# Kernel optimization log

Hardware: AMD Instinct MI355X
Metric: run time of the kernel (lower is better)

Reference implementation:

```python
import jax, jax.numpy as jnp
import numpy as np

N, D = 8192, 128
NOISEVAR = 1.0

def _softplusinverse(v):
    return np.log(1.0 - np.exp(-v)) + v

def setup_inputs() -> dict:
    key = jax.random.key(0)
    kx, kn = jax.random.split(key)
    x = jax.random.normal(kx, (N, D), dtype=jnp.float32)
    noise = jax.random.normal(kn, (N, D), dtype=jnp.float32)
    phi = jnp.asarray(_softplusinverse(NOISEVAR), dtype=jnp.float32)
    return {"x": x, "phi": phi, "noise": noise}

def reference(x, phi, noise):
    # x: [n, d] encoded features; phi: scalar noise param; noise: [n, d] i.i.d. N(0,1)
    n = x.shape[0]
    var = jax.nn.softplus(phi)
    # Pairwise squared L2 distances via Gram-matrix trick (same math as
    # norm(x_i - x_j)^2, avoids the [n, n, d] broadcast intermediate).
    sq = jnp.sum(x * x, axis=1)                                  # [n]
    d2 = jnp.maximum(sq[:, None] + sq[None, :] - 2.0 * (x @ x.T), 0.0)  # [n, n]
    kde_contribution = jnp.mean(jax.nn.logsumexp(-0.5 * d2 / var, axis=1))
    IXT_nats = jnp.log(jnp.float32(n)) - kde_contribution
    IXT = IXT_nats / jnp.log(jnp.float32(2.0))  # bits=True -> nats2bits
    out = x + var * noise                        # training=True noise injection
    return out, IXT
```

## Files before the change

### kernel.cpp

```cpp
#include <hip/hip_runtime.h>

#define N 8192
#define D 128
#define T64 64
#define NT64 (N / T64)
#define NPAIR (NT64 * (NT64 + 1) / 2)
#define PREFIX 2176
#define TBASE(t) ((t) * NT64 - ((t) * ((t) - 1)) / 2)

typedef __attribute__((ext_vector_type(4))) int intx4;
typedef unsigned long long u64;

static __device__ inline float softplus_of(const float* __restrict__ phi) {
    float p = phi[0];
    return (p > 20.f) ? p : log1pf(__expf(p));
}


__global__ __launch_bounds__(256) void k1_prep(
        const float* __restrict__ x, const float* __restrict__ phi,
        const float* __restrict__ noise, float* __restrict__ out,
        signed char* __restrict__ q8, int* __restrict__ sqv,
        float* __restrict__ rowsum) {
    int tid = threadIdx.x;
    int gid = blockIdx.x * 256 + tid;
    int row = gid >> 4;
    int gc  = gid & 15;

    const float* xs = x + (size_t)row * D + gc * 8;
    float4 u = *(const float4*)xs, v = *(const float4*)(xs + 4);

    float f[8] = {u.x, u.y, u.z, u.w, v.x, v.y, v.z, v.w};
    u64 pack = 0;
    int s = 0;
    #pragma unroll
    for (int k = 0; k < 8; k++) {
        float c = fminf(fmaxf(f[k] * 16.f, -127.f), 127.f);
        int q = (int)rintf(c);
        s += q * q;
        pack |= ((u64)(q & 255)) << (8 * k);
    }
    *(u64*)&q8[(size_t)row * D + gc * 8] = pack;

    #pragma unroll
    for (int m = 1; m < 16; m <<= 1) s += __shfl_xor(s, m, 64);
    if (gc == 0) { sqv[row] = s; rowsum[row] = 0.f; }

    if (row >= PREFIX) {
        float var = softplus_of(phi);
        const float* ns = noise + (size_t)row * D + gc * 8;
        float4 nu = *(const float4*)ns, nv = *(const float4*)(ns + 4);
        float4 o0, o1;
        o0.x = u.x + var * nu.x; o0.y = u.y + var * nu.y;
        o0.z = u.z + var * nu.z; o0.w = u.w + var * nu.w;
        o1.x = v.x + var * nv.x; o1.y = v.y + var * nv.y;
        o1.z = v.z + var * nv.z; o1.w = v.w + var * nv.w;
        float* od = out + (size_t)row * D + gc * 8;
        *(float4*)od = o0; *(float4*)(od + 4) = o1;
    }
}

__global__ __launch_bounds__(256, 4) void k2_gram(
        const signed char* __restrict__ q8, const float* __restrict__ phi,
        const int* __restrict__ sqv, float* __restrict__ rowsum) {
    const int tid  = threadIdx.x;
    const int w    = blockIdx.x * 4 + (tid >> 6);
    const int lane = tid & 63;
    const int lrow = lane & 15;
    const int quad = lane >> 4;

    const float fm = (float)(2 * NT64 + 1);
    int ti = (int)((fm - sqrtf(fm * fm - 8.0f * (float)w)) * 0.5f);
    while (TBASE(ti + 1) <= w) ++ti;
    while (TBASE(ti) > w) --ti;
    const int tj = ti + (w - TBASE(ti));

    const float var = softplus_of(phi);
    const float c2 = ((-0.5f / var) * 1.4426950408889634f) * (1.f / 256.f);
    const int Ts = (int)ceilf(30.f / (-c2));

    const int iB = ti * T64, jB = tj * T64;

    intx4 af[4][2], bf[4][2], sqi[4];
    int   sje[4];
    #pragma unroll
    for (int mt = 0; mt < 4; mt++) {
        const signed char* ar = q8 + (size_t)(iB + mt * 16 + lrow) * D + quad * 16;
        af[mt][0] = *(const intx4*)ar;
        af[mt][1] = *(const intx4*)(ar + 64);
    }
    #pragma unroll
    for (int nt = 0; nt < 4; nt++) {
        const signed char* br = q8 + (size_t)(jB + nt * 16 + lrow) * D + quad * 16;
        bf[nt][0] = *(const intx4*)br;
        bf[nt][1] = *(const intx4*)(br + 64);
    }
    #pragma unroll
    for (int mt = 0; mt < 4; mt++)
        sqi[mt] = *(const intx4*)&sqv[iB + mt * 16 + quad * 4];
    #pragma unroll
    for (int nt = 0; nt < 4; nt++)
        sje[nt] = sqv[jB + nt * 16 + lrow];

    #pragma unroll
    for (int nt = 0; nt < 4; nt++) {
        intx4 acc[4] = {};
        #pragma unroll
        for (int kk = 0; kk < 2; kk++)
            #pragma unroll
            for (int mt = 0; mt < 4; mt++)
                acc[mt] = __builtin_amdgcn_mfma_i32_16x16x64_i8(
                    af[mt][kk], bf[nt][kk], acc[mt], 0, 0, 0);

        const int sj = sje[nt];
        int mn = 0x7fffffff;
        #pragma unroll
        for (int mt = 0; mt < 4; mt++)
            #pragma unroll
            for (int reg = 0; reg < 4; reg++) {
                int d2s = sqi[mt][reg] + sj - (acc[mt][reg] << 1);
                mn = min(mn, d2s);
            }

        if (__any(mn < Ts)) {
            float colv = 0.f;
            #pragma unroll
            for (int mt = 0; mt < 4; mt++)
                #pragma unroll
                for (int reg = 0; reg < 4; reg++) {
                    int d2s = sqi[mt][reg] + sj - (acc[mt][reg] << 1);
                    float p = __builtin_amdgcn_exp2f((float)d2s * c2);
                    colv += p;
                    float rv = p;
                    rv += __shfl_xor(rv, 1, 64);
                    rv += __shfl_xor(rv, 2, 64);
                    rv += __shfl_xor(rv, 4, 64);
                    rv += __shfl_xor(rv, 8, 64);
                    if (lrow == 0)
                        atomicAdd(&rowsum[iB + mt * 16 + quad * 4 + reg], rv);
                }
            if (ti != tj) {
                colv += __shfl_xor(colv, 16, 64);
                colv += __shfl_xor(colv, 32, 64);
                if (quad == 0)
                    atomicAdd(&rowsum[jB + nt * 16 + lrow], colv);
            }
        }
    }
}

__global__ __launch_bounds__(256) void k4_out(
        const float* __restrict__ x, const float* __restrict__ phi,
        const float* __restrict__ noise, float* out,
        const float* __restrict__ rowsum) {
    const int tid = threadIdx.x;
    const float var = softplus_of(phi);

    if (blockIdx.x == 0) {
        __shared__ float red[4];
        float l = 0.f;
        #pragma unroll 4
        for (int i = tid; i < N; i += 256) l += logf(rowsum[i]);
        #pragma unroll
        for (int m = 1; m < 64; m <<= 1) l += __shfl_xor(l, m, 64);
        if ((tid & 63) == 0) red[tid >> 6] = l;
        __syncthreads();
        if (tid == 0) {
            float S = red[0] + red[1] + red[2] + red[3];
            float kde = S / (float)N;
            out[(size_t)N * D] =
                (logf((float)N) - kde) * 1.4426950408889634f;
        }
        __syncthreads();
        #pragma unroll
        for (int it = 0; it < 4; it++) {
            int idx = it * 256 + tid;
            size_t off = (size_t)2112 * D + idx * 8;
            const float* xs = x + off;
            const float* ns = noise + off;
            float4 u  = *(const float4*)xs, v  = *(const float4*)(xs + 4);
            float4 nu = *(const float4*)ns, nv = *(const float4*)(ns + 4);
            float4 o0, o1;
            o0.x = u.x + var * nu.x; o0.y = u.y + var * nu.y;
            o0.z = u.z + var * nu.z; o0.w = u.w + var * nu.w;
            o1.x = v.x + var * nv.x; o1.y = v.y + var * nv.y;
            o1.z = v.z + var * nv.z; o1.w = v.w + var * nv.w;
            float* od = out + off;
            *(float4*)od = o0; *(float4*)(od + 4) = o1;
        }
    } else {
        size_t gid = (size_t)(blockIdx.x - 1) * 256 + tid;
        const float* xs = x     + gid * 8;
        const float* ns = noise + gid * 8;
        float4 u  = *(const float4*)xs, v  = *(const float4*)(xs + 4);
        float4 nu = *(const float4*)ns, nv = *(const float4*)(ns + 4);
        float4 o0, o1;
        o0.x = u.x + var * nu.x; o0.y = u.y + var * nu.y;
        o0.z = u.z + var * nu.z; o0.w = u.w + var * nu.w;
        o1.x = v.x + var * nv.x; o1.y = v.y + var * nv.y;
        o1.z = v.z + var * nv.z; o1.w = v.w + var * nv.w;
        float* od = out + gid * 8;
        *(float4*)od = o0; *(float4*)(od + 4) = o1;
    }
}

extern "C" void kernel_launch(void* const* d_in, const int* in_sizes, int n_in,
                              void* d_out, int out_size, void* d_ws, size_t ws_size,
                              hipStream_t stream) {
    const float* x     = (const float*)d_in[0];
    const float* phi   = (const float*)d_in[1];
    const float* noise = (const float*)d_in[2];
    float* out = (float*)d_out;

    signed char* q8     = (signed char*)out;
    int*         sqv    = (int*)(out + (size_t)N * D / 4);
    float*       rowsum = (float*)(sqv + N);

    k1_prep<<<(N * 16) / 256, 256, 0, stream>>>(
        x, phi, noise, out, q8, sqv, rowsum);
    k2_gram<<<NPAIR / 4, 256, 0, stream>>>(q8, phi, sqv, rowsum);
    k4_out<<<1 + (2112 * 16) / 256, 256, 0, stream>>>(
        x, phi, noise, out, rowsum);
}
```

Baseline: 98.22 us.

## Process multiple tile pairs per wave with prefetch and block-min skip test

```diff
diff --git a/kernel.cpp b/kernel.cpp
--- a/kernel.cpp
+++ b/kernel.cpp
@@ -4,9 +4,8 @@
 #define D 128
 #define T64 64
 #define NT64 (N / T64)
-#define NPAIR (NT64 * (NT64 + 1) / 2)
-#define PREFIX 2176
-#define TBASE(t) ((t) * NT64 - ((t) * ((t) - 1)) / 2)
+#define PREFIX 2180
+#define K2BLK 768
 
 typedef __attribute__((ext_vector_type(4))) int intx4;
 typedef unsigned long long u64;
@@ -21,7 +20,8 @@
         const float* __restrict__ x, const float* __restrict__ phi,
         const float* __restrict__ noise, float* __restrict__ out,
         signed char* __restrict__ q8, int* __restrict__ sqv,
-        float* __restrict__ rowsum) {
+        float* __restrict__ rowsum, int* __restrict__ sqmin16) {
+    __shared__ int smin[16];
     int tid = threadIdx.x;
     int gid = blockIdx.x * 256 + tid;
     int row = gid >> 4;
@@ -44,7 +44,14 @@
 
     #pragma unroll
     for (int m = 1; m < 16; m <<= 1) s += __shfl_xor(s, m, 64);
-    if (gc == 0) { sqv[row] = s; rowsum[row] = 0.f; }
+    if (gc == 0) { sqv[row] = s; rowsum[row] = 0.f; smin[tid >> 4] = s; }
+    __syncthreads();
+    if (tid == 0) {
+        int m = smin[0];
+        #pragma unroll
+        for (int k = 1; k < 16; k++) m = min(m, smin[k]);
+        sqmin16[blockIdx.x] = m;
+    }
 
     if (row >= PREFIX) {
         float var = softplus_of(phi);
@@ -60,92 +67,117 @@
     }
 }
 
-__global__ __launch_bounds__(256, 4) void k2_gram(
+__global__ __launch_bounds__(256, 3) void k2_gram(
         const signed char* __restrict__ q8, const float* __restrict__ phi,
-        const int* __restrict__ sqv, float* __restrict__ rowsum) {
-    const int tid  = threadIdx.x;
-    const int w    = blockIdx.x * 4 + (tid >> 6);
-    const int lane = tid & 63;
+        const int* __restrict__ sqv, float* __restrict__ rowsum,
+        const int* __restrict__ sqmin16) {
+    const int w    = blockIdx.x * 4 + (threadIdx.x >> 6);
+    const int lane = threadIdx.x & 63;
     const int lrow = lane & 15;
     const int quad = lane >> 4;
 
-    const float fm = (float)(2 * NT64 + 1);
-    int ti = (int)((fm - sqrtf(fm * fm - 8.0f * (float)w)) * 0.5f);
-    while (TBASE(ti + 1) <= w) ++ti;
-    while (TBASE(ti) > w) --ti;
-    const int tj = ti + (w - TBASE(ti));
+    const int cnt = (w < 2112) ? 3 : 2;
+    int start     = (w < 2112) ? 3 * w : 2 * w + 2112;
+    int ti = 0, rem = start, len = NT64;
+    while (rem >= len) { rem -= len; ++ti; --len; }
+    int tj = ti + rem;
 
     const float var = softplus_of(phi);
     const float c2 = ((-0.5f / var) * 1.4426950408889634f) * (1.f / 256.f);
     const int Ts = (int)ceilf(30.f / (-c2));
 
-    const int iB = ti * T64, jB = tj * T64;
-
-    intx4 af[4][2], bf[4][2], sqi[4];
-    int   sje[4];
-    #pragma unroll
-    for (int mt = 0; mt < 4; mt++) {
-        const signed char* ar = q8 + (size_t)(iB + mt * 16 + lrow) * D + quad * 16;
-        af[mt][0] = *(const intx4*)ar;
-        af[mt][1] = *(const intx4*)(ar + 64);
-    }
+    intx4 af[4][2], bf[4][2];
+    int sqiMin = 0;
+    int curTi = -1;
+
     #pragma unroll
     for (int nt = 0; nt < 4; nt++) {
-        const signed char* br = q8 + (size_t)(jB + nt * 16 + lrow) * D + quad * 16;
+        const signed char* br = q8 + (size_t)(tj * T64 + nt * 16 + lrow) * D + quad * 16;
         bf[nt][0] = *(const intx4*)br;
         bf[nt][1] = *(const intx4*)(br + 64);
     }
-    #pragma unroll
-    for (int mt = 0; mt < 4; mt++)
-        sqi[mt] = *(const intx4*)&sqv[iB + mt * 16 + quad * 4];
-    #pragma unroll
-    for (int nt = 0; nt < 4; nt++)
-        sje[nt] = sqv[jB + nt * 16 + lrow];
-
-    #pragma unroll
-    for (int nt = 0; nt < 4; nt++) {
-        intx4 acc[4] = {};
-        #pragma unroll
-        for (int kk = 0; kk < 2; kk++)
+
+    for (int r = 0; r < cnt; ++r) {
+        const int iB = ti * T64, jB = tj * T64;
+
+        intx4 mj4 = *(const intx4*)&sqmin16[tj * 4];
+        const int sjMin = min(min(mj4[0], mj4[1]), min(mj4[2], mj4[3]));
+
+        if (ti != curTi) {
+            #pragma unroll
+            for (int mt = 0; mt < 4; mt++) {
+                const signed char* ar =
+                    q8 + (size_t)(iB + mt * 16 + lrow) * D + quad * 16;
+                af[mt][0] = *(const intx4*)ar;
+                af[mt][1] = *(const intx4*)(ar + 64);
+            }
+            intx4 mi4 = *(const intx4*)&sqmin16[ti * 4];
+            sqiMin = min(min(mi4[0], mi4[1]), min(mi4[2], mi4[3]));
+            curTi = ti;
+        }
+        const int Sthr = sqiMin + sjMin - Ts;
+
+        int nti = ti, ntj = tj + 1;
+        if (ntj == NT64) { ++nti; ntj = nti; }
+        const bool more = (r + 1 < cnt);
+
+        #pragma unroll
+        for (int nt = 0; nt < 4; nt++) {
+            intx4 acc[4] = {};
+            #pragma unroll
+            for (int kk = 0; kk < 2; kk++)
+                #pragma unroll
+                for (int mt = 0; mt < 4; mt++)
+                    acc[mt] = __builtin_amdgcn_mfma_i32_16x16x64_i8(
+                        af[mt][kk], bf[nt][kk], acc[mt], 0, 0, 0);
+
+            if (more) {
+                const signed char* br =
+                    q8 + (size_t)(ntj * T64 + nt * 16 + lrow) * D + quad * 16;
+                bf[nt][0] = *(const intx4*)br;
+                bf[nt][1] = *(const intx4*)(br + 64);
+            }
+
+            int mx = acc[0][0];
             #pragma unroll
             for (int mt = 0; mt < 4; mt++)
-                acc[mt] = __builtin_amdgcn_mfma_i32_16x16x64_i8(
-                    af[mt][kk], bf[nt][kk], acc[mt], 0, 0, 0);
-
-        const int sj = sje[nt];
-        int mn = 0x7fffffff;
-        #pragma unroll
-        for (int mt = 0; mt < 4; mt++)
-            #pragma unroll
-            for (int reg = 0; reg < 4; reg++) {
-                int d2s = sqi[mt][reg] + sj - (acc[mt][reg] << 1);
-                mn = min(mn, d2s);
-            }
-
-        if (__any(mn < Ts)) {
-            float colv = 0.f;
-            #pragma unroll
-            for (int mt = 0; mt < 4; mt++)
-                #pragma unroll
-                for (int reg = 0; reg < 4; reg++) {
-                    int d2s = sqi[mt][reg] + sj - (acc[mt][reg] << 1);
-                    float p = __builtin_amdgcn_exp2f((float)d2s * c2);
-                    colv += p;
-                    float rv = p;
-                    rv += __shfl_xor(rv, 1, 64);
-                    rv += __shfl_xor(rv, 2, 64);
-                    rv += __shfl_xor(rv, 4, 64);
-                    rv += __shfl_xor(rv, 8, 64);
-                    if (lrow == 0)
-                        atomicAdd(&rowsum[iB + mt * 16 + quad * 4 + reg], rv);
+                #pragma unroll
+                for (int reg = 0; reg < 4; reg++)
+                    mx = max(mx, acc[mt][reg]);
+
+            if (__any((mx << 1) > Sthr)) {
+                const int sj = sqv[jB + nt * 16 + lrow];
+                intx4 sqiv[4];
+                #pragma unroll
+                for (int mt = 0; mt < 4; mt++)
+                    sqiv[mt] = *(const intx4*)&sqv[iB + mt * 16 + quad * 4];
+
+                float colv = 0.f;
+                #pragma unroll
+                for (int mt = 0; mt < 4; mt++)
+                    #pragma unroll
+                    for (int reg = 0; reg < 4; reg++) {
+                        int d2s = sqiv[mt][reg] + sj - (acc[mt][reg] << 1);
+                        float p = __builtin_amdgcn_exp2f((float)d2s * c2);
+                        colv += p;
+                        float rv = p;
+                        rv += __shfl_xor(rv, 1, 64);
+                        rv += __shfl_xor(rv, 2, 64);
+                        rv += __shfl_xor(rv, 4, 64);
+                        rv += __shfl_xor(rv, 8, 64);
+                        if (lrow == 0)
+                            atomicAdd(&rowsum[iB + mt * 16 + quad * 4 + reg], rv);
+                    }
+                if (ti != tj) {
+                    colv += __shfl_xor(colv, 16, 64);
+                    colv += __shfl_xor(colv, 32, 64);
+                    if (quad == 0)
+                        atomicAdd(&rowsum[jB + nt * 16 + lrow], colv);
                 }
-            if (ti != tj) {
-                colv += __shfl_xor(colv, 16, 64);
-                colv += __shfl_xor(colv, 32, 64);
-                if (quad == 0)
-                    atomicAdd(&rowsum[jB + nt * 16 + lrow], colv);
-            }
-        }
+            }
+        }
+
+        ti = nti; tj = ntj;
     }
 }
 
@@ -173,20 +205,22 @@
         }
         __syncthreads();
         #pragma unroll
-        for (int it = 0; it < 4; it++) {
+        for (int it = 0; it < 5; it++) {
             int idx = it * 256 + tid;
-            size_t off = (size_t)2112 * D + idx * 8;
-            const float* xs = x + off;
-            const float* ns = noise + off;
-            float4 u  = *(const float4*)xs, v  = *(const float4*)(xs + 4);
-            float4 nu = *(const float4*)ns, nv = *(const float4*)(ns + 4);
-            float4 o0, o1;
-            o0.x = u.x + var * nu.x; o0.y = u.y + var * nu.y;
-            o0.z = u.z + var * nu.z; o0.w = u.w + var * nu.w;
-            o1.x = v.x + var * nv.x; o1.y = v.y + var * nv.y;
-            o1.z = v.z + var * nv.z; o1.w = v.w + var * nv.w;
-            float* od = out + off;
-            *(float4*)od = o0; *(float4*)(od + 4) = o1;
+            if (idx < (PREFIX - 2112) * 16) {
+                size_t off = (size_t)2112 * D + (size_t)idx * 8;
+                const float* xs = x + off;
+                const float* ns = noise + off;
+                float4 u  = *(const float4*)xs, v  = *(const float4*)(xs + 4);
+                float4 nu = *(const float4*)ns, nv = *(const float4*)(ns + 4);
+                float4 o0, o1;
+                o0.x = u.x + var * nu.x; o0.y = u.y + var * nu.y;
+                o0.z = u.z + var * nu.z; o0.w = u.w + var * nu.w;
+                o1.x = v.x + var * nv.x; o1.y = v.y + var * nv.y;
+                o1.z = v.z + var * nv.z; o1.w = v.w + var * nv.w;
+                float* od = out + off;
+                *(float4*)od = o0; *(float4*)(od + 4) = o1;
+            }
         }
     } else {
         size_t gid = (size_t)(blockIdx.x - 1) * 256 + tid;
@@ -212,13 +246,14 @@
     const float* noise = (const float*)d_in[2];
     float* out = (float*)d_out;
 
-    signed char* q8     = (signed char*)out;
-    int*         sqv    = (int*)(out + (size_t)N * D / 4);
-    float*       rowsum = (float*)(sqv + N);
+    signed char* q8      = (signed char*)out;
+    int*         sqv     = (int*)(out + (size_t)N * D / 4);
+    float*       rowsum  = (float*)(sqv + N);
+    int*         sqmin16 = (int*)(rowsum + N);
 
     k1_prep<<<(N * 16) / 256, 256, 0, stream>>>(
-        x, phi, noise, out, q8, sqv, rowsum);
-    k2_gram<<<NPAIR / 4, 256, 0, stream>>>(q8, phi, sqv, rowsum);
+        x, phi, noise, out, q8, sqv, rowsum, sqmin16);
+    k2_gram<<<K2BLK, 256, 0, stream>>>(q8, phi, sqv, rowsum, sqmin16);
     k4_out<<<1 + (2112 * 16) / 256, 256, 0, stream>>>(
         x, phi, noise, out, rowsum);
 }
```

Result: faster. 95.53 us (median of 2 runs) (-2.7%).
